# Performance work log

Hardware: AMD Instinct MI355X
Metric: run time of the kernel (lower is better)

Reference implementation:

```python
import math
import jax, jax.numpy as jnp
import numpy as np
from jax import lax

MUL_IN, MUL_OUT = 8, 16
DIM_IN, DIM_OUT = 4 * MUL_IN, 4 * MUL_OUT  # 0e(1) + 1o(3) per multiplicity
DIAMETER = 3.0
STEPS = (1.0, 1.0, 1.0)
NUM_RB = 4
BATCH, GRID = 8, 32


def _lattice():
    r = DIAMETER / 2
    axes = [np.arange(-math.floor(r / s), math.floor(r / s) + 1.0) * s for s in STEPS]
    return jnp.asarray(np.stack(np.meshgrid(*axes, indexing='ij'), axis=-1), jnp.float32)  # [X,Y,Z,3]


def _sus(x):
    # smooth unit step: exp(-1/x) for x>0 else 0
    return jnp.where(x > 0.0, jnp.exp(-1.0 / jnp.where(x > 0.0, x, 1.0)), 0.0)


def _radial_emb(lattice):
    # soft_one_hot_linspace, basis='smooth_finite', cutoff=True
    dist = jnp.linalg.norm(lattice, axis=-1)
    values = jnp.linspace(0.0, DIAMETER / 2, NUM_RB + 2)
    step = values[1] - values[0]
    diff = (dist[..., None] - values[1:-1]) / step
    return 1.14136 * jnp.exp(2.0) * _sus(diff + 1.0) * _sus(1.0 - diff)  # [X,Y,Z,NUM_RB]


def _sph(lattice):
    # real spherical harmonics l=0,1; normalize=True, 'component' normalization
    norm = jnp.linalg.norm(lattice, axis=-1, keepdims=True)
    unit = lattice / jnp.where(norm == 0.0, 1.0, norm)
    sh0 = jnp.ones(lattice.shape[:-1] + (1,), lattice.dtype)
    sh1 = jnp.sqrt(jnp.float32(3.0)) * unit
    return sh0, sh1


def setup_inputs() -> dict:
    key = jax.random.key(0)
    ks = jax.random.split(key, 7)
    x = jax.random.normal(ks[0], (BATCH, GRID, GRID, GRID, DIM_IN), jnp.float32)
    w_lin0 = jax.random.normal(ks[1], (MUL_IN, MUL_OUT), jnp.float32)
    w_lin1 = jax.random.normal(ks[2], (MUL_IN, MUL_OUT), jnp.float32)
    pshape = (NUM_RB, MUL_IN, 1, MUL_OUT)
    w000 = jax.random.normal(ks[3], pshape, jnp.float32)
    w011 = jax.random.normal(ks[4], pshape, jnp.float32)
    w101 = jax.random.normal(ks[5], pshape, jnp.float32)
    w110 = jax.random.normal(ks[6], pshape, jnp.float32)
    return dict(x=x, w_lin0=w_lin0, w_lin1=w_lin1, w000=w000, w011=w011, w101=w101, w110=w110)


def _forward(x, w_lin0, w_lin1, w000, w011, w101, w110):
    lattice = _lattice()
    emb = _radial_emb(lattice)
    sh0, sh1 = _sph(lattice)
    n_lat = lattice.shape[0] * lattice.shape[1] * lattice.shape[2]

    # ---- self-connection: FunctionalLinear(irreps_in -> irreps_out), per-l blocks ----
    lin_norm = 1.0 / math.sqrt(MUL_IN)
    x0 = x[..., :MUL_IN]                                             # [B,X,Y,Z,8]
    x1 = x[..., MUL_IN:].reshape(x.shape[:-1] + (MUL_IN, 3))         # [B,X,Y,Z,8,3]
    sc0 = jnp.einsum('...u,uw->...w', x0, w_lin0) * lin_norm
    sc1 = (jnp.einsum('...ui,uw->...wi', x1, w_lin1) * lin_norm).reshape(x.shape[:-1] + (3 * MUL_OUT,))
    sc = jnp.concatenate([sc0, sc1], axis=-1)                        # [B,X,Y,Z,DIM_OUT]

    # ---- radial weights per lattice point: einsum('xyzk,k...->xyz...') / n_lat ----
    def rad(w):
        return jnp.einsum('xyzk,kuvw->xyzuw', emb, w) / n_lat        # sh mul v == 1 squeezed
    r000, r011, r101, r110 = rad(w000), rad(w011), rad(w101), rad(w110)

    # ---- CG tensor-product 'right': build kernel [X,Y,Z, DIM_IN, DIM_OUT] ----
    inv_s3 = 1.0 / math.sqrt(3.0)  # w3j(0,1,1)=w3j(1,0,1)=w3j(1,1,0)=eye/sqrt(3); w3j(0,0,0)=1
    alpha = 1.0 / math.sqrt(2.0 * MUL_IN)  # 2 paths feed each output irrep, fan mul_in each

    eye3 = jnp.eye(3, dtype=x.dtype)
    # in 0e x sh 0e -> out 0e
    k00 = alpha * r000 * sh0[..., 0][..., None, None]                 # [X,Y,Z,8,16]
    # in 0e x sh 1o -> out 1o
    k01 = (alpha * inv_s3) * jnp.einsum('xyzuw,xyzm->xyzuwm', r011, sh1)
    k01 = k01.reshape(k01.shape[:3] + (MUL_IN, 3 * MUL_OUT))          # [X,Y,Z,8,48]
    # in 1o x sh 1o -> out 0e
    k10 = (alpha * inv_s3) * jnp.einsum('xyzuw,xyzi->xyzuiw', r110, sh1)
    k10 = k10.reshape(k10.shape[:3] + (3 * MUL_IN, MUL_OUT))          # [X,Y,Z,24,16]
    # in 1o x sh 0e -> out 1o
    k11 = (alpha * inv_s3) * jnp.einsum('xyzuw,im->xyzuiwm', r101 * sh0[..., 0][..., None, None], eye3)
    k11 = k11.reshape(k11.shape[:3] + (3 * MUL_IN, 3 * MUL_OUT))      # [X,Y,Z,24,48]

    k = jnp.concatenate([
        jnp.concatenate([k00, k01], axis=-1),
        jnp.concatenate([k10, k11], axis=-1),
    ], axis=-2)                                                       # [X,Y,Z,DIM_IN,DIM_OUT]

    conv = lax.conv_general_dilated(
        lhs=x, rhs=k, window_strides=(1, 1, 1), padding='SAME',
        dimension_numbers=('NXYZC', 'XYZIO', 'NXYZC'))
    return sc + conv


def reference(x, w_lin0, w_lin1, w000, w011, w101, w110):
    return _forward(x, w_lin0, w_lin1, w000, w011, w101, w110)
```

## Files before the change

### kernel.cpp

```cpp
#include <hip/hip_runtime.h>


typedef __attribute__((ext_vector_type(8))) short bf16x8;
typedef __attribute__((ext_vector_type(4))) float f32x4;

__device__ __forceinline__ float sus_f(float v) { return v > 0.f ? __expf(-1.f / v) : 0.f; }

__device__ __forceinline__ unsigned short f2bf(float f) {
    union { float f; unsigned u; } c; c.f = f;
    unsigned u = c.u;
    u += 0x7FFFu + ((u >> 16) & 1u);
    return (unsigned short)(u >> 16);
}

__global__ __launch_bounds__(256) void prep_k(
    const float* __restrict__ w_lin0, const float* __restrict__ w_lin1,
    const float* __restrict__ w000,  const float* __restrict__ w011,
    const float* __restrict__ w101,  const float* __restrict__ w110,
    unsigned short* __restrict__ kw)
{
    const int taps[19] = {1,3,4,5,7,9,10,11,12,13,14,15,16,17,19,21,22,23,25};
    const int ta = blockIdx.x;
    const int t = taps[ta];
    const int a = t / 9, b = (t / 3) % 3, c = t % 3;

    const float fx = (float)(a - 1), fy = (float)(b - 1), fz = (float)(c - 1);
    const float dist = sqrtf(fx * fx + fy * fy + fz * fz);
    float emb[4];
    #pragma unroll
    for (int r = 0; r < 4; ++r) {
        const float v = 0.3f * (float)(r + 1);
        const float d = (dist - v) * (1.0f / 0.3f);
        emb[r] = 8.4335731f * sus_f(d + 1.f) * sus_f(1.f - d);
    }
    const float s = (dist > 0.f) ? (1.7320508f / dist) : 0.f;
    const float shv[3] = { fx * s, fy * s, fz * s };
    const float S000 = 0.25f / 27.f;
    const float S1   = 0.25f * 0.57735027f / 27.f;
    const float LNRM = 0.35355339f;

    const int tid = threadIdx.x;
    const int ci = tid >> 3;

    #pragma unroll
    for (int j = 0; j < 8; ++j) {
        const int o = (tid & 7) * 8 + j;
        float val;
        if (ci < 8) {
            const int u = ci;
            if (o < 16) {
                const float* p = w000 + u * 16 + o;
                val = S000 * (emb[0]*p[0] + emb[1]*p[128] + emb[2]*p[256] + emb[3]*p[384]);
                if (t == 13) val += LNRM * w_lin0[u * 16 + o];
            } else {
                const int oo = o - 16, w = oo / 3, m = oo % 3;
                const float* p = w011 + u * 16 + w;
                val = S1 * shv[m] * (emb[0]*p[0] + emb[1]*p[128] + emb[2]*p[256] + emb[3]*p[384]);
            }
        } else {
            const int iu = ci - 8, u = iu / 3, ic = iu % 3;
            if (o < 16) {
                const float* p = w110 + u * 16 + o;
                val = S1 * shv[ic] * (emb[0]*p[0] + emb[1]*p[128] + emb[2]*p[256] + emb[3]*p[384]);
            } else {
                const int oo = o - 16, w = oo / 3, m = oo % 3;
                if (ic == m) {
                    const float* p = w101 + u * 16 + w;
                    val = S1 * (emb[0]*p[0] + emb[1]*p[128] + emb[2]*p[256] + emb[3]*p[384]);
                    if (t == 13) val += LNRM * w_lin1[u * 16 + w];
                } else {
                    val = 0.f;
                }
            }
        }
        const int g = ci >> 3, slot = ci & 7, nt = o >> 4, cc = o & 15;
        const int l = (g << 4) | cc;
        kw[((size_t)(ta * 4 + nt) * 64 + l) * 8 + slot] = f2bf(val);
    }
}

#define LXI(dx, y6, zp, ci) ((((dx) * 6 + (y6)) * 34 + (zp)) * 32 + (ci))

__global__ __launch_bounds__(256) void conv_mfma(
    const float* __restrict__ x,
    const unsigned short* __restrict__ kw,
    float* __restrict__ out)
{
    __shared__ unsigned short lx[3 * 6 * 34 * 32];

    const int bid = blockIdx.x;
    const int x8 = bid & 7;
    const int j  = bid >> 3;
    const int p  = x8 * 32 + (j >> 3);
    const int Yg = j & 7;
    const int n  = p >> 5;
    const int X  = p & 31;
    const int y0 = Yg * 4;
    const int tid = threadIdx.x;

    for (int r = tid; r < 576; r += 256) {
        const int dx = r / 192, rem = r - dx * 192;
        const int y6 = rem >> 5, z = rem & 31;
        const int gx = X + dx - 1, gy = y0 + y6 - 1;
        bf16x8 v[4];
        if ((unsigned)gx < 32u && (unsigned)gy < 32u) {
            const float4* sp = reinterpret_cast<const float4*>(
                x + ((size_t)(((n * 32 + gx) * 32 + gy) * 32 + z) << 5));
            #pragma unroll
            for (int q = 0; q < 4; ++q) {
                const float4 lo = sp[2 * q], hi = sp[2 * q + 1];
                bf16x8 w;
                w[0] = (short)f2bf(lo.x); w[1] = (short)f2bf(lo.y);
                w[2] = (short)f2bf(lo.z); w[3] = (short)f2bf(lo.w);
                w[4] = (short)f2bf(hi.x); w[5] = (short)f2bf(hi.y);
                w[6] = (short)f2bf(hi.z); w[7] = (short)f2bf(hi.w);
                v[q] = w;
            }
        } else {
            #pragma unroll
            for (int q = 0; q < 4; ++q) v[q] = (bf16x8)(short)0;
        }
        bf16x8* dp = reinterpret_cast<bf16x8*>(&lx[LXI(dx, y6, z + 1, 0)]);
        #pragma unroll
        for (int q = 0; q < 4; ++q) dp[q] = v[q];
    }
    if (tid < 36) {
        const int dxy = tid >> 1, zp = (tid & 1) * 33;
        bf16x8* dp = reinterpret_cast<bf16x8*>(&lx[(dxy * 34 + zp) * 32]);
        #pragma unroll
        for (int q = 0; q < 4; ++q) dp[q] = (bf16x8)(short)0;
    }
    __syncthreads();

    const int wid = tid >> 6;
    const int l   = tid & 63;
    const int lr  = l & 15;
    const int lg  = l >> 4;

    f32x4 acc[2][4];
    #pragma unroll
    for (int r = 0; r < 2; ++r)
        #pragma unroll
        for (int nt = 0; nt < 4; ++nt) acc[r][nt] = (f32x4)0.f;

    const bf16x8* kwf = reinterpret_cast<const bf16x8*>(kw);
    const int taps[19] = {1,3,4,5,7,9,10,11,12,13,14,15,16,17,19,21,22,23,25};

    #pragma unroll
    for (int ta = 0; ta < 19; ++ta) {
        const int t = taps[ta];
        const int a = t / 9, b = (t / 3) % 3, c = t % 3;

        bf16x8 bf[4];
        #pragma unroll
        for (int nt = 0; nt < 4; ++nt) bf[nt] = kwf[(size_t)(ta * 4 + nt) * 64 + l];

        #pragma unroll
        for (int r = 0; r < 2; ++r) {
            const bf16x8 af = *reinterpret_cast<const bf16x8*>(
                &lx[LXI(a, wid + b, 16 * r + lr + c, 8 * lg)]);
            #pragma unroll
            for (int nt = 0; nt < 4; ++nt)
                acc[r][nt] = __builtin_amdgcn_mfma_f32_16x16x32_bf16(af, bf[nt], acc[r][nt], 0, 0, 0);
        }
    }

    float* ob = out + ((size_t)(((n * 32 + X) * 32 + (y0 + wid)) * 32) << 6);
    #pragma unroll
    for (int r = 0; r < 2; ++r)
        #pragma unroll
        for (int nt = 0; nt < 4; ++nt)
            #pragma unroll
            for (int reg = 0; reg < 4; ++reg) {
                const int z = 16 * r + 4 * lg + reg;
                ob[((size_t)z << 6) + 16 * nt + lr] = acc[r][nt][reg];
            }
}

extern "C" void kernel_launch(void* const* d_in, const int* in_sizes, int n_in,
                              void* d_out, int out_size, void* d_ws, size_t ws_size,
                              hipStream_t stream) {
    const float* x    = (const float*)d_in[0];
    const float* wl0  = (const float*)d_in[1];
    const float* wl1  = (const float*)d_in[2];
    const float* w000 = (const float*)d_in[3];
    const float* w011 = (const float*)d_in[4];
    const float* w101 = (const float*)d_in[5];
    const float* w110 = (const float*)d_in[6];
    float* out = (float*)d_out;
    unsigned short* kw = (unsigned short*)d_ws;

    prep_k<<<dim3(19), dim3(256), 0, stream>>>(wl0, wl1, w000, w011, w101, w110, kw);
    conv_mfma<<<dim3(8 * 32 * 8), dim3(256), 0, stream>>>(x, kw, out);
}
```

Baseline: 51.41 us.

## Pre-convert input to swizzled bf16 and stage halo via direct global-to-LDS loads

Adds a separate pass that converts x to bf16 once into a workspace buffer, in an LDS-bank-swizzled layout. The convolution kernel can then copy halo rows straight into shared memory with global_load_lds instead of converting fp32 per block. Each block now computes 8 Y rows instead of 4, which cuts redundant halo reloads. Weight fragments are double-buffered across taps, and a fallback path keeps in-kernel conversion when the workspace is too small. The cost is an extra kernel launch and a full read and write of x in bf16, plus twice the accumulator registers per thread.

Measured after the change: 45.34 us. 11.8% less time.

```diff
diff --git a/kernel.cpp b/kernel.cpp
--- a/kernel.cpp
+++ b/kernel.cpp
@@ -3,6 +3,7 @@
 
 typedef __attribute__((ext_vector_type(8))) short bf16x8;
 typedef __attribute__((ext_vector_type(4))) float f32x4;
+typedef unsigned int u32;
 
 __device__ __forceinline__ float sus_f(float v) { return v > 0.f ? __expf(-1.f / v) : 0.f; }
 
@@ -74,107 +75,155 @@
             }
         }
         const int g = ci >> 3, slot = ci & 7, nt = o >> 4, cc = o & 15;
-        const int l = (g << 4) | cc;
-        kw[((size_t)(ta * 4 + nt) * 64 + l) * 8 + slot] = f2bf(val);
-    }
-}
-
-#define LXI(dx, y6, zp, ci) ((((dx) * 6 + (y6)) * 34 + (zp)) * 32 + (ci))
-
-__global__ __launch_bounds__(256) void conv_mfma(
+        const int lane = (g << 4) | cc;
+        kw[((size_t)(ta * 4 + nt) * 64 + lane) * 8 + slot] = f2bf(val);
+    }
+}
+
+__global__ __launch_bounds__(256) void xcvt(
+    const float* __restrict__ x, unsigned short* __restrict__ xb)
+{
+    const int gi = blockIdx.x * 256 + threadIdx.x;
+    const int vox = gi >> 2, g = gi & 3;
+    const int gz = vox & 31;
+    const float4* sp = reinterpret_cast<const float4*>(x) + (size_t)gi * 2;
+    const float4 lo = sp[0], hi = sp[1];
+    bf16x8 w;
+    w[0] = (short)f2bf(lo.x); w[1] = (short)f2bf(lo.y);
+    w[2] = (short)f2bf(lo.z); w[3] = (short)f2bf(lo.w);
+    w[4] = (short)f2bf(hi.x); w[5] = (short)f2bf(hi.y);
+    w[6] = (short)f2bf(hi.z); w[7] = (short)f2bf(hi.w);
+    const int slot = g ^ (((gz + 1) >> 1) & 3);
+    const size_t dst = ((size_t)(vox >> 5) << 10) + (gz << 5) + (slot << 3);
+    *reinterpret_cast<bf16x8*>(xb + dst) = w;
+}
+
+template<bool DIRECT>
+__global__ __launch_bounds__(256, 2) void conv_mfma(
     const float* __restrict__ x,
+    const unsigned short* __restrict__ xb,
     const unsigned short* __restrict__ kw,
     float* __restrict__ out)
 {
-    __shared__ unsigned short lx[3 * 6 * 34 * 32];
-
+    __shared__ unsigned short lx[3 * 10 * 34 * 32];
+
+    const int tid = threadIdx.x;
     const int bid = blockIdx.x;
-    const int x8 = bid & 7;
-    const int j  = bid >> 3;
-    const int p  = x8 * 32 + (j >> 3);
-    const int Yg = j & 7;
-    const int n  = p >> 5;
-    const int X  = p & 31;
-    const int y0 = Yg * 4;
-    const int tid = threadIdx.x;
-
-    for (int r = tid; r < 576; r += 256) {
-        const int dx = r / 192, rem = r - dx * 192;
-        const int y6 = rem >> 5, z = rem & 31;
-        const int gx = X + dx - 1, gy = y0 + y6 - 1;
-        bf16x8 v[4];
-        if ((unsigned)gx < 32u && (unsigned)gy < 32u) {
-            const float4* sp = reinterpret_cast<const float4*>(
-                x + ((size_t)(((n * 32 + gx) * 32 + gy) * 32 + z) << 5));
-            #pragma unroll
-            for (int q = 0; q < 4; ++q) {
-                const float4 lo = sp[2 * q], hi = sp[2 * q + 1];
-                bf16x8 w;
-                w[0] = (short)f2bf(lo.x); w[1] = (short)f2bf(lo.y);
-                w[2] = (short)f2bf(lo.z); w[3] = (short)f2bf(lo.w);
-                w[4] = (short)f2bf(hi.x); w[5] = (short)f2bf(hi.y);
-                w[6] = (short)f2bf(hi.z); w[7] = (short)f2bf(hi.w);
-                v[q] = w;
-            }
-        } else {
-            #pragma unroll
-            for (int q = 0; q < 4; ++q) v[q] = (bf16x8)(short)0;
-        }
-        bf16x8* dp = reinterpret_cast<bf16x8*>(&lx[LXI(dx, y6, z + 1, 0)]);
-        #pragma unroll
-        for (int q = 0; q < 4; ++q) dp[q] = v[q];
-    }
-    if (tid < 36) {
-        const int dxy = tid >> 1, zp = (tid & 1) * 33;
-        bf16x8* dp = reinterpret_cast<bf16x8*>(&lx[(dxy * 34 + zp) * 32]);
-        #pragma unroll
-        for (int q = 0; q < 4; ++q) dp[q] = (bf16x8)(short)0;
+    const int xcd = bid & 7, idx = bid >> 3;
+    const int gid = xcd * 128 + idx;
+    const int n = gid >> 7, X = (gid >> 2) & 31, Yg = gid & 3;
+    const int Y0 = Yg * 8;
+    const int wid = tid >> 6, l = tid & 63, lr = l & 15, lg = l >> 4;
+
+    f32x4* lz = reinterpret_cast<f32x4*>(lx);
+    #pragma unroll
+    for (int i = 0; i < 16; ++i) {
+        const int j = tid + i * 256;
+        if (j < 4080) lz[j] = (f32x4)0.f;
     }
     __syncthreads();
 
-    const int wid = tid >> 6;
-    const int l   = tid & 63;
-    const int lr  = l & 15;
-    const int lg  = l >> 4;
-
-    f32x4 acc[2][4];
-    #pragma unroll
-    for (int r = 0; r < 2; ++r)
+    if (DIRECT) {
+        #pragma unroll
+        for (int k = 0; k < 8; ++k) {
+            const int rr = wid + (k << 2);
+            if (rr < 30) {
+                const int dx = rr / 10, y6 = rr - dx * 10;
+                const int gx = X + dx - 1, gy = Y0 + y6 - 1;
+                if ((unsigned)gx < 32u && (unsigned)gy < 32u) {
+                    const char* src = reinterpret_cast<const char*>(xb) +
+                        ((size_t)((n * 32 + gx) * 32 + gy) << 11);
+                    char* dstrow = reinterpret_cast<char*>(lx) + rr * 2176 + 64;
+                    __builtin_amdgcn_global_load_lds(
+                        (const __attribute__((address_space(1))) u32*)(src + l * 16),
+                        (__attribute__((address_space(3))) u32*)(dstrow), 16, 0, 0);
+                    __builtin_amdgcn_global_load_lds(
+                        (const __attribute__((address_space(1))) u32*)(src + 1024 + l * 16),
+                        (__attribute__((address_space(3))) u32*)(dstrow + 1024), 16, 0, 0);
+                }
+            }
+        }
+    } else {
+        for (int it = tid; it < 960; it += 256) {
+            const int dx = it / 320, rem = it - dx * 320;
+            const int y6 = rem >> 5, z = rem & 31;
+            const int gx = X + dx - 1, gy = Y0 + y6 - 1;
+            if ((unsigned)gx < 32u && (unsigned)gy < 32u) {
+                const float4* sp = reinterpret_cast<const float4*>(
+                    x + ((size_t)(((n * 32 + gx) * 32 + gy) * 32 + z) << 5));
+                const int swz = ((z + 1) >> 1) & 3;
+                char* row = reinterpret_cast<char*>(lx) + (dx * 10 + y6) * 2176 + (z + 1) * 64;
+                #pragma unroll
+                for (int g = 0; g < 4; ++g) {
+                    const float4 lo = sp[2 * g], hi = sp[2 * g + 1];
+                    bf16x8 w;
+                    w[0] = (short)f2bf(lo.x); w[1] = (short)f2bf(lo.y);
+                    w[2] = (short)f2bf(lo.z); w[3] = (short)f2bf(lo.w);
+                    w[4] = (short)f2bf(hi.x); w[5] = (short)f2bf(hi.y);
+                    w[6] = (short)f2bf(hi.z); w[7] = (short)f2bf(hi.w);
+                    *reinterpret_cast<bf16x8*>(row + ((g ^ swz) << 4)) = w;
+                }
+            }
+        }
+    }
+    __syncthreads();
+
+    constexpr int TA[19] = {1,3,4,5,7,9,10,11,12,13,14,15,16,17,19,21,22,23,25};
+    const bf16x8* kwf = reinterpret_cast<const bf16x8*>(kw);
+    const char* lxc = reinterpret_cast<const char*>(lx);
+    const int yloc = wid * 2;
+
+    f32x4 acc[4][4];
+    #pragma unroll
+    for (int r = 0; r < 4; ++r)
         #pragma unroll
         for (int nt = 0; nt < 4; ++nt) acc[r][nt] = (f32x4)0.f;
 
-    const bf16x8* kwf = reinterpret_cast<const bf16x8*>(kw);
-    const int taps[19] = {1,3,4,5,7,9,10,11,12,13,14,15,16,17,19,21,22,23,25};
+    bf16x8 bcur[4];
+    #pragma unroll
+    for (int nt = 0; nt < 4; ++nt) bcur[nt] = kwf[(size_t)nt * 64 + l];
 
     #pragma unroll
     for (int ta = 0; ta < 19; ++ta) {
-        const int t = taps[ta];
+        const int t = TA[ta];
         const int a = t / 9, b = (t / 3) % 3, c = t % 3;
 
-        bf16x8 bf[4];
-        #pragma unroll
-        for (int nt = 0; nt < 4; ++nt) bf[nt] = kwf[(size_t)(ta * 4 + nt) * 64 + l];
-
-        #pragma unroll
-        for (int r = 0; r < 2; ++r) {
-            const bf16x8 af = *reinterpret_cast<const bf16x8*>(
-                &lx[LXI(a, wid + b, 16 * r + lr + c, 8 * lg)]);
+        bf16x8 bnext[4];
+        if (ta < 18) {
             #pragma unroll
             for (int nt = 0; nt < 4; ++nt)
-                acc[r][nt] = __builtin_amdgcn_mfma_f32_16x16x32_bf16(af, bf[nt], acc[r][nt], 0, 0, 0);
-        }
-    }
-
-    float* ob = out + ((size_t)(((n * 32 + X) * 32 + (y0 + wid)) * 32) << 6);
-    #pragma unroll
-    for (int r = 0; r < 2; ++r)
+                bnext[nt] = kwf[(size_t)((ta + 1) * 4 + nt) * 64 + l];
+        }
+
+        #pragma unroll
+        for (int r = 0; r < 4; ++r) {
+            const int y10 = yloc + (r >> 1) + b;
+            const int zp = 16 * (r & 1) + lr + c;
+            const int byte = ((a * 10 + y10) * 34 + zp) * 64 + ((lg ^ ((zp >> 1) & 3)) << 4);
+            const bf16x8 af = *reinterpret_cast<const bf16x8*>(lxc + byte);
+            #pragma unroll
+            for (int nt = 0; nt < 4; ++nt)
+                acc[r][nt] = __builtin_amdgcn_mfma_f32_16x16x32_bf16(af, bcur[nt], acc[r][nt], 0, 0, 0);
+        }
+
+        if (ta < 18) {
+            #pragma unroll
+            for (int nt = 0; nt < 4; ++nt) bcur[nt] = bnext[nt];
+        }
+    }
+
+    float* ob = out + ((size_t)(((n * 32 + X) * 32 + Y0 + yloc) * 32) << 6);
+    #pragma unroll
+    for (int r = 0; r < 4; ++r) {
+        float* oy = ob + (size_t)(r >> 1) * 2048;
         #pragma unroll
         for (int nt = 0; nt < 4; ++nt)
             #pragma unroll
             for (int reg = 0; reg < 4; ++reg) {
-                const int z = 16 * r + 4 * lg + reg;
-                ob[((size_t)z << 6) + 16 * nt + lr] = acc[r][nt][reg];
-            }
+                const int z = 16 * (r & 1) + 4 * lg + reg;
+                oy[z * 64 + nt * 16 + lr] = acc[r][nt][reg];
+            }
+    }
 }
 
 extern "C" void kernel_launch(void* const* d_in, const int* in_sizes, int n_in,
@@ -188,8 +237,18 @@
     const float* w101 = (const float*)d_in[5];
     const float* w110 = (const float*)d_in[6];
     float* out = (float*)d_out;
+
     unsigned short* kw = (unsigned short*)d_ws;
+    const size_t KWB = 77824;
+    const size_t XBB = 16777216ull;
 
     prep_k<<<dim3(19), dim3(256), 0, stream>>>(wl0, wl1, w000, w011, w101, w110, kw);
-    conv_mfma<<<dim3(8 * 32 * 8), dim3(256), 0, stream>>>(x, kw, out);
-}
+
+    if (ws_size >= KWB + XBB) {
+        unsigned short* xb = (unsigned short*)((char*)d_ws + KWB);
+        xcvt<<<dim3(4096), dim3(256), 0, stream>>>(x, xb);
+        conv_mfma<true><<<dim3(1024), dim3(256), 0, stream>>>(x, xb, kw, out);
+    } else {
+        conv_mfma<false><<<dim3(1024), dim3(256), 0, stream>>>(x, nullptr, kw, out);
+    }
+}
```
